# Performance work log

Measured on AMD Instinct MI355X. Metric: run time of the kernel, lower is better.

The kernel has to match this reference:

```python
import jax, jax.numpy as jnp
import numpy as np

B, T, N, E = 16, 24, 300, 9600
H, F = 3, 8            # num_heads, out_feats of EdgeGAT
GRU_H = 16
NUM_AIRPORTS, HORIZON = 300, 24
NEG_SLOPE = 0.2


def setup_inputs() -> dict:
    key = jax.random.key(0)
    ks = jax.random.split(key, 16)
    s = 0.1
    x = jax.random.normal(ks[0], (B, T, N, 1), jnp.float32)
    edge_weight = jax.random.uniform(ks[1], (B, T, E, 1), jnp.float32)
    src = jax.random.randint(ks[2], (E,), 0, N)
    dst = jax.random.randint(ks[3], (E,), 0, N)
    W_node = jax.random.normal(ks[4], (1, H * F), jnp.float32) * s
    W_edge = jax.random.normal(ks[5], (1, H * F), jnp.float32) * s
    attn_l = jax.random.normal(ks[6], (H, F), jnp.float32) * s
    attn_r = jax.random.normal(ks[7], (H, F), jnp.float32) * s
    attn_e = jax.random.normal(ks[8], (H, F), jnp.float32) * s
    gat_bias = jax.random.normal(ks[9], (H * F,), jnp.float32) * s
    W_ih = jax.random.normal(ks[10], (3 * GRU_H, H * F), jnp.float32) * s
    W_hh = jax.random.normal(ks[11], (3 * GRU_H, GRU_H), jnp.float32) * s
    b_ih = jax.random.normal(ks[12], (3 * GRU_H,), jnp.float32) * s
    b_hh = jax.random.normal(ks[13], (3 * GRU_H,), jnp.float32) * s
    W_fc = jax.random.normal(ks[14], (NUM_AIRPORTS * HORIZON, GRU_H), jnp.float32) * s
    b_fc = jax.random.normal(ks[15], (NUM_AIRPORTS * HORIZON,), jnp.float32) * s
    return dict(x=x, edge_weight=edge_weight, W_node=W_node, W_edge=W_edge,
                attn_l=attn_l, attn_r=attn_r, attn_e=attn_e, gat_bias=gat_bias,
                W_ih=W_ih, W_hh=W_hh, b_ih=b_ih, b_hh=b_hh,
                W_fc=W_fc, b_fc=b_fc, src=src, dst=dst)


def _forward(x, edge_weight, W_node, W_edge, attn_l, attn_r, attn_e, gat_bias,
             W_ih, W_hh, b_ih, b_hh, W_fc, b_fc, src, dst):
    # --- EdgeGAT on all B*T graphs at once (shared topology, varying feats) ---
    feat = (x @ W_node).reshape(B, T, N, H, F)            # [B,T,N,H,F]
    fe = (edge_weight @ W_edge).reshape(B, T, E, H, F)    # [B,T,E,H,F]
    el = jnp.einsum('btnhf,hf->btnh', feat, attn_l)       # [B,T,N,H]
    er = jnp.einsum('btnhf,hf->btnh', feat, attn_r)
    ee = jnp.einsum('btehf,hf->bteh', fe, attn_e)
    e = jax.nn.leaky_relu(el[:, :, src] + er[:, :, dst] + ee, NEG_SLOPE)  # [B,T,E,H]
    # edge softmax over incoming edges of each dst node
    e_t = jnp.moveaxis(e, 2, 0)                           # [E,B,T,H]
    m = jax.ops.segment_max(e_t, dst, num_segments=N)     # [N,B,T,H]
    num = jnp.exp(e_t - m[dst])
    den = jax.ops.segment_sum(num, dst, num_segments=N)
    alpha = num / den[dst]                                # [E,B,T,H]
    ft_src = jnp.moveaxis(feat[:, :, src], 2, 0)          # [E,B,T,H,F]
    rst = jax.ops.segment_sum(ft_src * alpha[..., None], dst, num_segments=N)  # [N,B,T,H,F]
    rst = rst.reshape(N, B, T, H * F) + gat_bias          # bias of EdgeGATConv
    # mean-pool over nodes per graph -> GRU input sequence
    gru_in = rst.mean(axis=0)                             # [B,T,24]
    # --- GRU (torch semantics), return final hidden state ---
    def step(h, xt):
        gi = xt @ W_ih.T + b_ih
        gh = h @ W_hh.T + b_hh
        i_r, i_z, i_n = jnp.split(gi, 3, axis=-1)
        h_r, h_z, h_n = jnp.split(gh, 3, axis=-1)
        r = jax.nn.sigmoid(i_r + h_r)
        z = jax.nn.sigmoid(i_z + h_z)
        n = jnp.tanh(i_n + r * h_n)
        return (1.0 - z) * n + z * h, None
    h0 = jnp.zeros((B, GRU_H), gru_in.dtype)
    h_n, _ = jax.lax.scan(step, h0, jnp.moveaxis(gru_in, 1, 0))  # scan over T
    return h_n @ W_fc.T + b_fc                            # [B, num_airports*horizon]


def reference(x, edge_weight, W_node, W_edge, attn_l, attn_r, attn_e, gat_bias,
              W_ih, W_hh, b_ih, b_hh, W_fc, b_fc, src, dst):
    return _forward(x, edge_weight, W_node, W_edge, attn_l, attn_r, attn_e, gat_bias,
                    W_ih, W_hh, b_ih, b_hh, W_fc, b_fc, src, dst)
```

## Files before the change

### kernel.cpp

```cpp
#include <hip/hip_runtime.h>
#include <math.h>

#define B_ 16
#define T_ 24
#define G_ 384
#define N_ 300
#define E_ 9600
#define H_ 3
#define F_ 8
#define HF_ 24
#define GRUH_ 16
#define OUTB_ 7200
#define NW_ 16
#define TPB_ 640

__global__ __launch_bounds__(1024) void csr_kernel(
    const int* __restrict__ src, const int* __restrict__ dst,
    int* __restrict__ rp, unsigned* __restrict__ pk)
{
    __shared__ int cnt[NW_ * N_];
    __shared__ int tot[N_];
    __shared__ int rps[N_ + 1];
    const int tid = threadIdx.x;
    const int w = tid >> 6;

    for (int i = tid; i < NW_ * N_; i += 1024) cnt[i] = 0;
    __syncthreads();
    for (int i = tid; i < E_; i += 1024) atomicAdd(&cnt[w * N_ + dst[i]], 1);
    __syncthreads();
    if (tid < N_) {
        int run = 0;
        #pragma unroll
        for (int k = 0; k < NW_; ++k) {
            int t = cnt[k * N_ + tid];
            cnt[k * N_ + tid] = run;
            run += t;
        }
        tot[tid] = run;
    }
    __syncthreads();
    if (tid < 64) {
        int base = 0;
        for (int c = 0; c < 5; ++c) {
            int i = c * 64 + tid;
            int orig = (i < N_) ? tot[i] : 0;
            int v = orig;
            #pragma unroll
            for (int o = 1; o < 64; o <<= 1) {
                int u = __shfl_up(v, o, 64);
                if (tid >= o) v += u;
            }
            if (i < N_) rps[i] = base + v - orig;
            base += __shfl(v, 63, 64);
        }
        if (tid == 0) rps[N_] = base;
    }
    __syncthreads();
    for (int i = tid; i <= N_; i += 1024) rp[i] = rps[i];
    for (int i = tid; i < E_; i += 1024) {
        int d = dst[i];
        int pos = rps[d] + atomicAdd(&cnt[w * N_ + d], 1);
        pk[pos] = (unsigned)i | ((unsigned)src[i] << 17);
    }
}

__global__ __launch_bounds__(TPB_) void gat_kernel(
    const float* __restrict__ x, const float* __restrict__ ew,
    const float* __restrict__ Wn, const float* __restrict__ We,
    const float* __restrict__ al, const float* __restrict__ ar,
    const float* __restrict__ ae,
    const int* __restrict__ rp_g, const unsigned* __restrict__ pk_g,
    float* __restrict__ S)
{
    __shared__ float ews[E_];
    __shared__ unsigned pkl[E_];
    __shared__ float xs[N_];
    __shared__ int rp_l[N_ + 1];
    __shared__ float cf[9];
    __shared__ float Sred[10][3];

    const int g = blockIdx.x;
    const int tid = threadIdx.x;
    const long base_e = (long)g * E_;

    const float4* ew4 = (const float4*)(ew + base_e);
    float4* ews4 = (float4*)ews;
    for (int i = tid; i < E_ / 4; i += TPB_) ews4[i] = ew4[i];
    const uint4* pk4 = (const uint4*)pk_g;
    uint4* pkl4 = (uint4*)pkl;
    for (int i = tid; i < E_ / 4; i += TPB_) pkl4[i] = pk4[i];
    for (int i = tid; i < N_; i += TPB_) xs[i] = x[g * N_ + i];
    for (int i = tid; i <= N_; i += TPB_) rp_l[i] = rp_g[i];
    if (tid < H_) {
        int h = tid;
        float cl = 0.f, cr = 0.f, ce = 0.f;
        #pragma unroll
        for (int f = 0; f < F_; ++f) {
            float wn = Wn[h * F_ + f];
            cl += wn * al[h * F_ + f];
            cr += wn * ar[h * F_ + f];
            ce += We[h * F_ + f] * ae[h * F_ + f];
        }
        cf[h] = cl; cf[3 + h] = cr; cf[6 + h] = ce;
    }
    __syncthreads();

    float n0 = 0.f, d0 = 0.f, n1 = 0.f, d1 = 0.f, n2 = 0.f, d2 = 0.f;
    if (tid < 2 * N_) {
        const int n = tid >> 1;
        const int half = tid & 1;
        const float xd = xs[n];
        const float c0l = cf[0], c1l = cf[1], c2l = cf[2];
        const float c0r = cf[3], c1r = cf[4], c2r = cf[5];
        const float c0e = cf[6], c1e = cf[7], c2e = cf[8];
        const int p1 = rp_l[n + 1];
        for (int p = rp_l[n] + half; p < p1; p += 2) {
            unsigned pkv = pkl[p];
            float w = ews[pkv & 0x1FFFFu];
            float xsv = xs[pkv >> 17];
            float e0 = fmaf(xsv, c0l, fmaf(xd, c0r, w * c0e)); e0 = e0 > 0.f ? e0 : 0.2f * e0;
            float e1 = fmaf(xsv, c1l, fmaf(xd, c1r, w * c1e)); e1 = e1 > 0.f ? e1 : 0.2f * e1;
            float e2 = fmaf(xsv, c2l, fmaf(xd, c2r, w * c2e)); e2 = e2 > 0.f ? e2 : 0.2f * e2;
            float p0 = __expf(e0), pe1 = __expf(e1), pe2 = __expf(e2);
            d0 += p0;  n0 += p0 * xsv;
            d1 += pe1; n1 += pe1 * xsv;
            d2 += pe2; n2 += pe2 * xsv;
        }
    }
    n0 += __shfl_xor(n0, 1); d0 += __shfl_xor(d0, 1);
    n1 += __shfl_xor(n1, 1); d1 += __shfl_xor(d1, 1);
    n2 += __shfl_xor(n2, 1); d2 += __shfl_xor(d2, 1);
    float a0 = 0.f, a1 = 0.f, a2 = 0.f;
    if (tid < 2 * N_ && (tid & 1) == 0) {
        a0 = d0 > 0.f ? n0 / d0 : 0.f;
        a1 = d1 > 0.f ? n1 / d1 : 0.f;
        a2 = d2 > 0.f ? n2 / d2 : 0.f;
    }
    for (int o = 32; o; o >>= 1) {
        a0 += __shfl_down(a0, o);
        a1 += __shfl_down(a1, o);
        a2 += __shfl_down(a2, o);
    }
    const int wave = tid >> 6, lane = tid & 63;
    if (lane == 0) { Sred[wave][0] = a0; Sred[wave][1] = a1; Sred[wave][2] = a2; }
    __syncthreads();
    if (tid < 3) {
        float s = 0.f;
        #pragma unroll
        for (int w2 = 0; w2 < TPB_ / 64; ++w2) s += Sred[w2][tid];
        S[g * 3 + tid] = s;
    }
}

__global__ __launch_bounds__(256) void fc_kernel(
    const float* __restrict__ S, const float* __restrict__ Wn,
    const float* __restrict__ gb, const float* __restrict__ Wih,
    const float* __restrict__ bih, const float* __restrict__ Whh,
    const float* __restrict__ bhh, const float* __restrict__ Wfc,
    const float* __restrict__ bfc, float* __restrict__ out)
{
    __shared__ float S2[2][T_][H_];
    __shared__ float hS[2][GRUH_];
    const int tid = threadIdx.x;
    const int idx0 = blockIdx.x * 256;
    const int b0 = idx0 / OUTB_;

    if (tid < 2 * T_ * H_) {
        const int grp = tid / (T_ * H_);
        const int rem = tid - grp * (T_ * H_);
        const int t = rem / H_, h = rem - t * H_;
        const int bb = b0 + grp;
        float s = 0.f;
        if (bb < B_) s = S[(bb * T_ + t) * H_ + h];
        S2[grp][t][h] = s * (1.0f / N_);
    }
    __syncthreads();

    if (tid < 64) {
        const int grp = tid >> 4;
        const int u = tid & 15;
        const int gbase = tid & ~15;
        const bool active = (grp < 2) && (b0 + grp < B_);
        const int sgrp = active ? grp : 0;

        float whr[GRUH_], whz[GRUH_], whn[GRUH_];
        #pragma unroll
        for (int k = 0; k < GRUH_; ++k) {
            whr[k] = Whh[u * GRUH_ + k];
            whz[k] = Whh[(16 + u) * GRUH_ + k];
            whn[k] = Whh[(32 + u) * GRUH_ + k];
        }
        const float bhr = bhh[u], bhz = bhh[16 + u], bhn = bhh[32 + u];

        float A[3][3], C[3];
        #pragma unroll
        for (int r = 0; r < 3; ++r) {
            const int j = r * 16 + u;
            float cc = bih[j];
            A[r][0] = A[r][1] = A[r][2] = 0.f;
            #pragma unroll
            for (int k = 0; k < HF_; ++k) {
                float wk = Wih[j * HF_ + k];
                cc += wk * gb[k];
                A[r][k >> 3] += wk * Wn[k];
            }
            C[r] = cc;
        }

        float h = 0.f;
        for (int t = 0; t < T_; ++t) {
            float S0 = S2[sgrp][t][0], S1 = S2[sgrp][t][1], Sv2 = S2[sgrp][t][2];
            float gr = C[0] + A[0][0] * S0 + A[0][1] * S1 + A[0][2] * Sv2;
            float gz = C[1] + A[1][0] * S0 + A[1][1] * S1 + A[1][2] * Sv2;
            float gn = C[2] + A[2][0] * S0 + A[2][1] * S1 + A[2][2] * Sv2;
            float hr = bhr, hz = bhz, hn = bhn;
            #pragma unroll
            for (int k = 0; k < GRUH_; ++k) {
                float hk = __shfl(h, gbase + k, 64);
                hr += whr[k] * hk;
                hz += whz[k] * hk;
                hn += whn[k] * hk;
            }
            float r = 1.f / (1.f + __expf(-(gr + hr)));
            float z = 1.f / (1.f + __expf(-(gz + hz)));
            float nn = tanhf(gn + r * hn);
            h = (1.f - z) * nn + z * h;
        }
        if (active) hS[grp][u] = h;
    }
    __syncthreads();

    const int idx = idx0 + tid;
    if (idx < B_ * OUTB_) {
        const int b = idx / OUTB_, o = idx - b * OUTB_;
        const float4* wr = (const float4*)(Wfc + (long)o * GRUH_);
        const float* hr = hS[b - b0];
        float4 w0 = wr[0], w1 = wr[1], w2 = wr[2], w3 = wr[3];
        float acc = bfc[o];
        acc += hr[0]  * w0.x + hr[1]  * w0.y + hr[2]  * w0.z + hr[3]  * w0.w;
        acc += hr[4]  * w1.x + hr[5]  * w1.y + hr[6]  * w1.z + hr[7]  * w1.w;
        acc += hr[8]  * w2.x + hr[9]  * w2.y + hr[10] * w2.z + hr[11] * w2.w;
        acc += hr[12] * w3.x + hr[13] * w3.y + hr[14] * w3.z + hr[15] * w3.w;
        out[idx] = acc;
    }
}

extern "C" void kernel_launch(void* const* d_in, const int* in_sizes, int n_in,
                              void* d_out, int out_size, void* d_ws, size_t ws_size,
                              hipStream_t stream) {
    const float* x    = (const float*)d_in[0];
    const float* ew   = (const float*)d_in[1];
    const float* Wn   = (const float*)d_in[2];
    const float* We   = (const float*)d_in[3];
    const float* al   = (const float*)d_in[4];
    const float* ar   = (const float*)d_in[5];
    const float* ae   = (const float*)d_in[6];
    const float* gb   = (const float*)d_in[7];
    const float* Wih  = (const float*)d_in[8];
    const float* Whh  = (const float*)d_in[9];
    const float* bih  = (const float*)d_in[10];
    const float* bhh  = (const float*)d_in[11];
    const float* Wfc  = (const float*)d_in[12];
    const float* bfc  = (const float*)d_in[13];
    const int*   src  = (const int*)d_in[14];
    const int*   dst  = (const int*)d_in[15];
    float* out = (float*)d_out;

    int* rp = (int*)d_ws;
    unsigned* pk = (unsigned*)(rp + 320);
    float* S = (float*)(pk + E_);

    csr_kernel<<<1, 1024, 0, stream>>>(src, dst, rp, pk);
    gat_kernel<<<G_, TPB_, 0, stream>>>(x, ew, Wn, We, al, ar, ae, rp, pk, S);
    fc_kernel<<<(B_ * OUTB_ + 255) / 256, 256, 0, stream>>>(S, Wn, gb, Wih, bih,
                                                            Whh, bhh, Wfc, bfc, out);
}
```

Baseline: 43.80 us.

## Fuse CSR construction into GAT kernel and gather edge weights from global

```diff
diff --git a/kernel.cpp b/kernel.cpp
--- a/kernel.cpp
+++ b/kernel.cpp
@@ -11,27 +11,52 @@
 #define HF_ 24
 #define GRUH_ 16
 #define OUTB_ 7200
-#define NW_ 16
 #define TPB_ 640
-
-__global__ __launch_bounds__(1024) void csr_kernel(
+#define NWC_ 10
+
+__global__ __launch_bounds__(TPB_) void gat_kernel(
+    const float* __restrict__ x, const float* __restrict__ ew,
+    const float* __restrict__ Wn, const float* __restrict__ We,
+    const float* __restrict__ al, const float* __restrict__ ar,
+    const float* __restrict__ ae,
     const int* __restrict__ src, const int* __restrict__ dst,
-    int* __restrict__ rp, unsigned* __restrict__ pk)
+    float* __restrict__ S)
 {
-    __shared__ int cnt[NW_ * N_];
+    __shared__ unsigned pkl[E_];
+    __shared__ int cnt[NWC_ * N_];
     __shared__ int tot[N_];
     __shared__ int rps[N_ + 1];
+    __shared__ float xs[N_];
+    __shared__ float cf[9];
+    __shared__ float Sred[NWC_][3];
+
+    const int g = blockIdx.x;
     const int tid = threadIdx.x;
     const int w = tid >> 6;
-
-    for (int i = tid; i < NW_ * N_; i += 1024) cnt[i] = 0;
-    __syncthreads();
-    for (int i = tid; i < E_; i += 1024) atomicAdd(&cnt[w * N_ + dst[i]], 1);
+    const long base_e = (long)g * E_;
+
+    for (int i = tid; i < N_; i += TPB_) xs[i] = x[g * N_ + i];
+    if (tid < H_) {
+        int h = tid;
+        float cl = 0.f, cr = 0.f, ce = 0.f;
+        #pragma unroll
+        for (int f = 0; f < F_; ++f) {
+            float wn = Wn[h * F_ + f];
+            cl += wn * al[h * F_ + f];
+            cr += wn * ar[h * F_ + f];
+            ce += We[h * F_ + f] * ae[h * F_ + f];
+        }
+        cf[h] = cl; cf[3 + h] = cr; cf[6 + h] = ce;
+    }
+
+    for (int i = tid; i < NWC_ * N_; i += TPB_) cnt[i] = 0;
+    __syncthreads();
+    for (int i = tid; i < E_; i += TPB_) atomicAdd(&cnt[w * N_ + dst[i]], 1);
     __syncthreads();
     if (tid < N_) {
         int run = 0;
         #pragma unroll
-        for (int k = 0; k < NW_; ++k) {
+        for (int k = 0; k < NWC_; ++k) {
             int t = cnt[k * N_ + tid];
             cnt[k * N_ + tid] = run;
             run += t;
@@ -56,52 +81,10 @@
         if (tid == 0) rps[N_] = base;
     }
     __syncthreads();
-    for (int i = tid; i <= N_; i += 1024) rp[i] = rps[i];
-    for (int i = tid; i < E_; i += 1024) {
+    for (int i = tid; i < E_; i += TPB_) {
         int d = dst[i];
         int pos = rps[d] + atomicAdd(&cnt[w * N_ + d], 1);
-        pk[pos] = (unsigned)i | ((unsigned)src[i] << 17);
-    }
-}
-
-__global__ __launch_bounds__(TPB_) void gat_kernel(
-    const float* __restrict__ x, const float* __restrict__ ew,
-    const float* __restrict__ Wn, const float* __restrict__ We,
-    const float* __restrict__ al, const float* __restrict__ ar,
-    const float* __restrict__ ae,
-    const int* __restrict__ rp_g, const unsigned* __restrict__ pk_g,
-    float* __restrict__ S)
-{
-    __shared__ float ews[E_];
-    __shared__ unsigned pkl[E_];
-    __shared__ float xs[N_];
-    __shared__ int rp_l[N_ + 1];
-    __shared__ float cf[9];
-    __shared__ float Sred[10][3];
-
-    const int g = blockIdx.x;
-    const int tid = threadIdx.x;
-    const long base_e = (long)g * E_;
-
-    const float4* ew4 = (const float4*)(ew + base_e);
-    float4* ews4 = (float4*)ews;
-    for (int i = tid; i < E_ / 4; i += TPB_) ews4[i] = ew4[i];
-    const uint4* pk4 = (const uint4*)pk_g;
-    uint4* pkl4 = (uint4*)pkl;
-    for (int i = tid; i < E_ / 4; i += TPB_) pkl4[i] = pk4[i];
-    for (int i = tid; i < N_; i += TPB_) xs[i] = x[g * N_ + i];
-    for (int i = tid; i <= N_; i += TPB_) rp_l[i] = rp_g[i];
-    if (tid < H_) {
-        int h = tid;
-        float cl = 0.f, cr = 0.f, ce = 0.f;
-        #pragma unroll
-        for (int f = 0; f < F_; ++f) {
-            float wn = Wn[h * F_ + f];
-            cl += wn * al[h * F_ + f];
-            cr += wn * ar[h * F_ + f];
-            ce += We[h * F_ + f] * ae[h * F_ + f];
-        }
-        cf[h] = cl; cf[3 + h] = cr; cf[6 + h] = ce;
+        pkl[pos] = (unsigned)i | ((unsigned)src[i] << 17);
     }
     __syncthreads();
 
@@ -113,14 +96,14 @@
         const float c0l = cf[0], c1l = cf[1], c2l = cf[2];
         const float c0r = cf[3], c1r = cf[4], c2r = cf[5];
         const float c0e = cf[6], c1e = cf[7], c2e = cf[8];
-        const int p1 = rp_l[n + 1];
-        for (int p = rp_l[n] + half; p < p1; p += 2) {
+        const int p1 = rps[n + 1];
+        for (int p = rps[n] + half; p < p1; p += 2) {
             unsigned pkv = pkl[p];
-            float w = ews[pkv & 0x1FFFFu];
+            float wv = ew[base_e + (pkv & 0x1FFFFu)];
             float xsv = xs[pkv >> 17];
-            float e0 = fmaf(xsv, c0l, fmaf(xd, c0r, w * c0e)); e0 = e0 > 0.f ? e0 : 0.2f * e0;
-            float e1 = fmaf(xsv, c1l, fmaf(xd, c1r, w * c1e)); e1 = e1 > 0.f ? e1 : 0.2f * e1;
-            float e2 = fmaf(xsv, c2l, fmaf(xd, c2r, w * c2e)); e2 = e2 > 0.f ? e2 : 0.2f * e2;
+            float e0 = fmaf(xsv, c0l, fmaf(xd, c0r, wv * c0e)); e0 = e0 > 0.f ? e0 : 0.2f * e0;
+            float e1 = fmaf(xsv, c1l, fmaf(xd, c1r, wv * c1e)); e1 = e1 > 0.f ? e1 : 0.2f * e1;
+            float e2 = fmaf(xsv, c2l, fmaf(xd, c2r, wv * c2e)); e2 = e2 > 0.f ? e2 : 0.2f * e2;
             float p0 = __expf(e0), pe1 = __expf(e1), pe2 = __expf(e2);
             d0 += p0;  n0 += p0 * xsv;
             d1 += pe1; n1 += pe1 * xsv;
@@ -147,7 +130,7 @@
     if (tid < 3) {
         float s = 0.f;
         #pragma unroll
-        for (int w2 = 0; w2 < TPB_ / 64; ++w2) s += Sred[w2][tid];
+        for (int w2 = 0; w2 < NWC_; ++w2) s += Sred[w2][tid];
         S[g * 3 + tid] = s;
     }
 }
@@ -223,7 +206,9 @@
             }
             float r = 1.f / (1.f + __expf(-(gr + hr)));
             float z = 1.f / (1.f + __expf(-(gz + hz)));
-            float nn = tanhf(gn + r * hn);
+            float xa = gn + r * hn;
+            float te = __expf(-2.f * xa);
+            float nn = (1.f - te) / (1.f + te);
             h = (1.f - z) * nn + z * h;
         }
         if (active) hS[grp][u] = h;
@@ -266,12 +251,9 @@
     const int*   dst  = (const int*)d_in[15];
     float* out = (float*)d_out;
 
-    int* rp = (int*)d_ws;
-    unsigned* pk = (unsigned*)(rp + 320);
-    float* S = (float*)(pk + E_);
-
-    csr_kernel<<<1, 1024, 0, stream>>>(src, dst, rp, pk);
-    gat_kernel<<<G_, TPB_, 0, stream>>>(x, ew, Wn, We, al, ar, ae, rp, pk, S);
+    float* S = (float*)d_ws;
+
+    gat_kernel<<<G_, TPB_, 0, stream>>>(x, ew, Wn, We, al, ar, ae, src, dst, S);
     fc_kernel<<<(B_ * OUTB_ + 255) / 256, 256, 0, stream>>>(S, Wn, gb, Wih, bih,
                                                             Whh, bhh, Wfc, bfc, out);
 }
```

Measured after the change: 35.51 us, median of 2. -18.9%, faster.
